# Kernel tuning notes

Hardware: AMD Instinct MI355X
Metric: run time of the kernel (lower is better)

The kernel has to match this reference:

```python
import math
import jax, jax.numpy as jnp
import numpy as np

NH = 16          # num_attention_heads
MAX_REL = 512    # max_relative_positions


def _t4(x):
    # [B, N, H] -> [B, NH, N, H/NH]  (transpose_for_scores)
    B, N, H = x.shape
    return x.reshape(B, N, NH, -1).transpose(0, 2, 1, 3)


def setup_inputs() -> dict:
    key = jax.random.key(0)
    ks = jax.random.split(key, 6)
    B, N, H = 1, 2048, 1024
    hidden_states = jax.random.normal(ks[0], (B, N, H), jnp.float32)
    attention_mask = jnp.ones((B, 1, N, N), jnp.int32)
    ids = jnp.arange(N, dtype=jnp.int32)
    relative_pos = ids[:, None] - ids[None, :]              # [N, N], build_relative_position
    rel_embeddings = jax.random.normal(ks[1], (2 * MAX_REL, H), jnp.float32) * 0.02
    in_proj_w = jax.random.normal(ks[2], (3 * H, H), jnp.float32) * 0.02
    q_bias = jnp.zeros((H,), jnp.float32)
    v_bias = jnp.zeros((H,), jnp.float32)
    pos_proj_w = jax.random.normal(ks[3], (H, H), jnp.float32) * 0.02
    pos_q_proj_w = jax.random.normal(ks[4], (H, H), jnp.float32) * 0.02
    pos_q_proj_b = jnp.zeros((H,), jnp.float32)
    return dict(hidden_states=hidden_states, attention_mask=attention_mask,
                relative_pos=relative_pos, rel_embeddings=rel_embeddings,
                in_proj_w=in_proj_w, q_bias=q_bias, v_bias=v_bias,
                pos_proj_w=pos_proj_w, pos_q_proj_w=pos_q_proj_w,
                pos_q_proj_b=pos_q_proj_b)


def reference(hidden_states, attention_mask, relative_pos, rel_embeddings,
              in_proj_w, q_bias, v_bias, pos_proj_w, pos_q_proj_w, pos_q_proj_b):
    B, N, H = hidden_states.shape
    dh = H // NH
    scale_factor = 1 + 2  # 1 + len(["c2p", "p2c"])
    scale = math.sqrt(dh * scale_factor)

    # fused QKV projection; chunk(3, dim=-1) AFTER transpose_for_scores -> per-head q|k|v layout
    qp = hidden_states @ in_proj_w.T                          # [B, N, 3H]
    q, k, v = jnp.split(_t4(qp), 3, axis=-1)                  # each [B, NH, N, dh]
    q = q + _t4(q_bias[None, None, :])
    v = v + _t4(v_bias[None, None, :])
    q = q / scale

    scores = jnp.einsum('bhqd,bhkd->bhqk', q, k)              # content-content

    # disentangled relative-position bias
    span = min(N, MAX_REL)                                    # att_span
    rel = rel_embeddings[MAX_REL - span:MAX_REL + span][None] # [1, 2S, H]
    rpos = relative_pos.astype(jnp.int32)[None, None]         # [1, 1, N, N]

    # c2p: content-to-position
    pos_k = _t4(rel @ pos_proj_w.T)                           # [1, NH, 2S, dh]
    c2p = jnp.einsum('bhqd,xhsd->bhqs', q, pos_k)             # [B, NH, N, 2S]
    c2p_pos = jnp.clip(rpos + span, 0, 2 * span - 1)
    c2p = jnp.take_along_axis(c2p, c2p_pos, axis=-1)          # gather -> [B, NH, N, N]

    # p2c: position-to-content
    pos_q = _t4(rel @ pos_q_proj_w.T + pos_q_proj_b) / scale  # [1, NH, 2S, dh]
    p2c = jnp.einsum('bhkd,xhsd->bhks', k, pos_q)             # [B, NH, N, 2S]
    p2c_pos = jnp.clip(-rpos + span, 0, 2 * span - 1)
    p2c = jnp.take_along_axis(p2c, p2c_pos, axis=-1)          # [B, NH, K, Q]
    p2c = jnp.swapaxes(p2c, -1, -2)                           # -> [B, NH, Q, K]

    scores = scores + c2p + p2c

    # XSoftmax: masked softmax, masked probs zeroed
    m = attention_mask.astype(bool)                           # [B, 1, N, N]
    probs = jax.nn.softmax(jnp.where(m, scores, -jnp.inf), axis=-1)
    probs = jnp.where(m, probs, 0.0)

    ctx = jnp.einsum('bhqk,bhkd->bhqd', probs, v)             # [B, NH, N, dh]
    return ctx.transpose(0, 2, 1, 3).reshape(B, N, H)
```

## Files before the change

### kernel.cpp

```cpp
#include <hip/hip_runtime.h>
#include <hip/hip_bf16.h>

typedef __bf16 bf16;
typedef __attribute__((ext_vector_type(8))) __bf16 bf16x8;
typedef __attribute__((ext_vector_type(8))) float f32x8;
typedef __attribute__((ext_vector_type(4))) float f32x4;

#define MFMA(a,b,c) __builtin_amdgcn_mfma_f32_16x16x32_bf16((a),(b),(c),0,0,0)

__device__ __forceinline__ bf16x8 ld8(const bf16* p){ bf16x8 v; __builtin_memcpy(&v,p,16); return v; }
__device__ __forceinline__ void   st8(bf16* p, bf16x8 v){ __builtin_memcpy(p,&v,16); }

__global__ __launch_bounds__(256)
void cvt_kernel(const float* __restrict__ s0, const float* __restrict__ s1,
                const float* __restrict__ s2, const float* __restrict__ s3,
                const float* __restrict__ s4,
                bf16* d0, bf16* d1, bf16* d2, bf16* d3, bf16* d4)
{
    const int sizes[5] = {2097152, 3145728, 1048576, 1048576, 1048576};
    const float* s; bf16* d;
    switch (blockIdx.y) {
        case 0: s = s0; d = d0; break;  case 1: s = s1; d = d1; break;
        case 2: s = s2; d = d2; break;  case 3: s = s3; d = d3; break;
        default: s = s4; d = d4;
    }
    const int n = sizes[blockIdx.y];
    const int stride = gridDim.x * 256 * 8;
    for (int i = (blockIdx.x * 256 + threadIdx.x) * 8; i < n; i += stride) {
        f32x8 v; __builtin_memcpy(&v, s + i, 32);
        bf16x8 r;
        #pragma unroll
        for (int j = 0; j < 8; j++) r[j] = (bf16)v[j];
        st8(d + i, r);
    }
}

__global__ __launch_bounds__(256)
void gemm_stage(const bf16* __restrict__ A, const bf16* __restrict__ Bpk,
                const bf16* __restrict__ Bpq, int K, int mode,
                const float* __restrict__ qb, const float* __restrict__ vb,
                bf16* __restrict__ o0, bf16* __restrict__ o1, bf16* __restrict__ o2,
                float* __restrict__ part)
{
    __shared__ __attribute__((aligned(16))) bf16 As[128][32];
    __shared__ __attribute__((aligned(16))) bf16 Bs[128][32];

    const int tid = threadIdx.x, w = tid >> 6, lane = tid & 63;
    const int l15 = lane & 15, quad = lane >> 4;
    const int wr = w >> 1, wc = w & 1;

    int arr = 0, my = blockIdx.y, kbeg = 0, kend = K;
    const bf16* B = Bpk;
    if (mode == 1) {
        arr = my >> 3; my &= 7;
        B = arr ? Bpq : Bpk;
        kbeg = blockIdx.z * 256; kend = kbeg + 256;
    }
    const int m0 = my * 128, n0 = blockIdx.x * 128;
    const int srow = tid >> 2, scol = (tid & 3) * 8;

    f32x4 acc[4][4] = {};
    for (int k0 = kbeg; k0 < kend; k0 += 32) {
        __syncthreads();
        st8(&As[srow][scol],    ld8(A + (size_t)(m0 + srow) * K + k0 + scol));
        st8(&As[srow+64][scol], ld8(A + (size_t)(m0 + 64 + srow) * K + k0 + scol));
        st8(&Bs[srow][scol],    ld8(B + (size_t)(n0 + srow) * K + k0 + scol));
        st8(&Bs[srow+64][scol], ld8(B + (size_t)(n0 + 64 + srow) * K + k0 + scol));
        __syncthreads();
        bf16x8 a[4], b[4];
        #pragma unroll
        for (int i = 0; i < 4; i++) a[i] = ld8(&As[wr*64 + i*16 + l15][quad*8]);
        #pragma unroll
        for (int j = 0; j < 4; j++) b[j] = ld8(&Bs[wc*64 + j*16 + l15][quad*8]);
        #pragma unroll
        for (int i = 0; i < 4; i++)
            #pragma unroll
            for (int j = 0; j < 4; j++)
                acc[i][j] = MFMA(a[i], b[j], acc[i][j]);
    }

    const float inv_scale = 0.07216878364870323f;
    #pragma unroll
    for (int i = 0; i < 4; i++) {
        #pragma unroll
        for (int j = 0; j < 4; j++) {
            #pragma unroll
            for (int r = 0; r < 4; r++) {
                int row = m0 + wr*64 + i*16 + quad*4 + r;
                int col = n0 + wc*64 + j*16 + l15;
                float v = acc[i][j][r];
                if (mode == 0) {
                    int h = col / 192, rr = col % 192;
                    if (rr < 64)
                        o0[((size_t)h*2048 + row)*64 + rr] =
                            (bf16)((v + qb[h*64 + rr]) * inv_scale);
                    else if (rr < 128)
                        o1[((size_t)h*2048 + row)*64 + (rr - 64)] = (bf16)v;
                    else
                        o2[((size_t)h*64 + (rr - 128))*2048 + row] =
                            (bf16)(v + vb[h*64 + (rr - 128)]);
                } else {
                    part[(((size_t)(arr*4 + blockIdx.z)*1024 + row)*1024) + col] = v;
                }
            }
        }
    }
}

__global__ __launch_bounds__(256)
void pos_merge(const float* __restrict__ part, const float* __restrict__ pqb,
               bf16* __restrict__ PKw, bf16* __restrict__ PQw)
{
    int e = blockIdx.x * 256 + threadIdx.x;
    int arr = e >> 20, r = (e >> 10) & 1023, c = e & 1023;
    const float* p = part + ((size_t)arr*4) * 1048576 + (size_t)r * 1024 + c;
    float v = p[0] + p[1048576] + p[2*1048576] + p[3*1048576];
    int h = c >> 6, d = c & 63;
    if (arr == 0) PKw[((size_t)h*1024 + r)*64 + d] = (bf16)v;
    else          PQw[((size_t)h*1024 + r)*64 + d] =
                      (bf16)((v + pqb[c]) * 0.07216878364870323f);
}

__global__ __launch_bounds__(256)
void edge_kernel(const bf16* __restrict__ Qw, const bf16* __restrict__ Kw,
                 const bf16* __restrict__ PKw, const bf16* __restrict__ PQw,
                 float* __restrict__ C2Pe, float* __restrict__ P2Ce)
{
    int t = blockIdx.x * 256 + threadIdx.x;
    int side = t >> 15, rest = t & 32767;
    int h = rest >> 11, n = rest & 2047;
    const bf16* row = (side ? Kw : Qw) + ((size_t)h*2048 + n) * 64;
    const bf16* eb  = (side ? PQw : PKw) + (size_t)h*1024*64;
    float a0 = 0.f, a1 = 0.f;
    #pragma unroll
    for (int c = 0; c < 8; c++) {
        bf16x8 x  = ld8(row + c*8);
        bf16x8 e0 = ld8(eb + c*8);
        bf16x8 e1 = ld8(eb + (size_t)1023*64 + c*8);
        #pragma unroll
        for (int j = 0; j < 8; j++) {
            a0 += (float)x[j] * (float)e0[j];
            a1 += (float)x[j] * (float)e1[j];
        }
    }
    float* o = side ? P2Ce : C2Pe;
    o[((size_t)h*2048 + n)*2 + 0] = a0;
    o[((size_t)h*2048 + n)*2 + 1] = a1;
}

__global__ __launch_bounds__(64, 2)
void attn_kernel(const bf16* __restrict__ Q, const bf16* __restrict__ Kc,
                 const bf16* __restrict__ Vt, const bf16* __restrict__ PK,
                 const bf16* __restrict__ PQ,
                 const float* __restrict__ C2Pe, const float* __restrict__ P2Ce,
                 float* __restrict__ out)
{
    __shared__ bf16 W1s[16][82];
    __shared__ bf16 W2s[64][82];
    __shared__ __attribute__((aligned(16))) bf16 Ps[16][72];

    const int lane = threadIdx.x;
    const int l15 = lane & 15, quad = lane >> 4;
    const int h = blockIdx.y, qw0 = blockIdx.x * 16;

    const bf16* Qh  = Q  + (size_t)h * 2048 * 64;
    const bf16* Kh  = Kc + (size_t)h * 2048 * 64;
    const bf16* Vh  = Vt + (size_t)h * 64 * 2048;
    const bf16* PKh = PK + (size_t)h * 1024 * 64;
    const bf16* PQh = PQ + (size_t)h * 1024 * 64;

    bf16x8 qa[2];
    #pragma unroll
    for (int s = 0; s < 2; s++)
        qa[s] = ld8(Qh + (size_t)(qw0 + l15)*64 + s*32 + quad*8);

    float c2pe0[4], c2pe1[4];
    #pragma unroll
    for (int r = 0; r < 4; r++) {
        int q = qw0 + quad*4 + r;
        c2pe0[r] = C2Pe[((size_t)h*2048 + q)*2 + 0];
        c2pe1[r] = C2Pe[((size_t)h*2048 + q)*2 + 1];
    }

    f32x4 oacc[4] = {};
    float psum[4] = {0.f, 0.f, 0.f, 0.f};

    for (int kb = 0; kb < 32; kb++) {
        const int k0 = kb * 64;

        bf16x8 kf[4][2];
        #pragma unroll
        for (int nt = 0; nt < 4; nt++)
            #pragma unroll
            for (int s = 0; s < 2; s++)
                kf[nt][s] = ld8(Kh + (size_t)(k0 + nt*16 + l15)*64 + s*32 + quad*8);

        f32x4 sacc[4] = {};
        #pragma unroll
        for (int s = 0; s < 2; s++)
            #pragma unroll
            for (int nt = 0; nt < 4; nt++)
                sacc[nt] = MFMA(qa[s], kf[nt][s], sacc[nt]);

        float val[4][4];
        if (k0 >= qw0 + 527) {
            float p2[4];
            #pragma unroll
            for (int nt = 0; nt < 4; nt++)
                p2[nt] = P2Ce[((size_t)h*2048 + k0 + nt*16 + l15)*2 + 0];
            #pragma unroll
            for (int nt = 0; nt < 4; nt++)
                #pragma unroll
                for (int r = 0; r < 4; r++)
                    val[nt][r] = sacc[nt][r] + c2pe0[r] + p2[nt];
        } else if (k0 <= qw0 - 574) {
            float p2[4];
            #pragma unroll
            for (int nt = 0; nt < 4; nt++)
                p2[nt] = P2Ce[((size_t)h*2048 + k0 + nt*16 + l15)*2 + 1];
            #pragma unroll
            for (int nt = 0; nt < 4; nt++)
                #pragma unroll
                for (int r = 0; r < 4; r++)
                    val[nt][r] = sacc[nt][r] + c2pe1[r] + p2[nt];
        } else {
            const int winb = qw0 - k0 + 449;
            {
                f32x4 a1[5] = {};
                #pragma unroll
                for (int s = 0; s < 2; s++)
                    #pragma unroll
                    for (int n5 = 0; n5 < 5; n5++) {
                        int c = winb + n5*16 + l15;
                        c = min(max(c, 0), 1023);
                        bf16x8 bq = ld8(PKh + (size_t)c*64 + s*32 + quad*8);
                        a1[n5] = MFMA(qa[s], bq, a1[n5]);
                    }
                #pragma unroll
                for (int n5 = 0; n5 < 5; n5++)
                    #pragma unroll
                    for (int r = 0; r < 4; r++)
                        W1s[quad*4 + r][n5*16 + l15] = (bf16)a1[n5][r];
            }
            {
                bf16x8 pq[5][2];
                #pragma unroll
                for (int s = 0; s < 2; s++)
                    #pragma unroll
                    for (int n5 = 0; n5 < 5; n5++) {
                        int c = winb + n5*16 + l15;
                        c = min(max(c, 0), 1023);
                        pq[n5][s] = ld8(PQh + (size_t)c*64 + s*32 + quad*8);
                    }
                #pragma unroll
                for (int mt = 0; mt < 4; mt++) {
                    f32x4 a2[5] = {};
                    #pragma unroll
                    for (int s = 0; s < 2; s++)
                        #pragma unroll
                        for (int n5 = 0; n5 < 5; n5++)
                            a2[n5] = MFMA(kf[mt][s], pq[n5][s], a2[n5]);
                    #pragma unroll
                    for (int n5 = 0; n5 < 5; n5++)
                        #pragma unroll
                        for (int r = 0; r < 4; r++)
                            W2s[mt*16 + quad*4 + r][n5*16 + l15] = (bf16)a2[n5][r];
                }
            }
            #pragma unroll
            for (int nt = 0; nt < 4; nt++)
                #pragma unroll
                for (int r = 0; r < 4; r++) {
                    int off = quad*4 + r - nt*16 - l15 + 63;
                    val[nt][r] = sacc[nt][r] + (float)W1s[quad*4 + r][off]
                                             + (float)W2s[nt*16 + l15][off];
                }
        }

        #pragma unroll
        for (int nt = 0; nt < 4; nt++)
            #pragma unroll
            for (int r = 0; r < 4; r++) {
                float e = __expf(val[nt][r]);
                psum[r] += e;
                Ps[quad*4 + r][nt*16 + l15] = (bf16)e;
            }

        #pragma unroll
        for (int s = 0; s < 2; s++) {
            bf16x8 pa = ld8(&Ps[l15][s*32 + quad*8]);
            #pragma unroll
            for (int dt = 0; dt < 4; dt++) {
                bf16x8 vf = ld8(Vh + (size_t)(dt*16 + l15)*2048 + k0 + s*32 + quad*8);
                oacc[dt] = MFMA(pa, vf, oacc[dt]);
            }
        }
    }

    #pragma unroll
    for (int r = 0; r < 4; r++)
        #pragma unroll
        for (int m = 1; m < 16; m <<= 1)
            psum[r] += __shfl_xor(psum[r], m);
    #pragma unroll
    for (int dt = 0; dt < 4; dt++)
        #pragma unroll
        for (int r = 0; r < 4; r++) {
            int row = qw0 + quad*4 + r;
            out[(size_t)row*1024 + h*64 + dt*16 + l15] = oacc[dt][r] / psum[r];
        }
}

extern "C" void kernel_launch(void* const* d_in, const int* in_sizes, int n_in,
                              void* d_out, int out_size, void* d_ws, size_t ws_size,
                              hipStream_t stream)
{
    (void)in_sizes; (void)n_in; (void)out_size; (void)ws_size;
    const float* X   = (const float*)d_in[0];
    const float* REL = (const float*)d_in[3];
    const float* Win = (const float*)d_in[4];
    const float* qb  = (const float*)d_in[5];
    const float* vb  = (const float*)d_in[6];
    const float* Wpk = (const float*)d_in[7];
    const float* Wpq = (const float*)d_in[8];
    const float* pqb = (const float*)d_in[9];
    float* out = (float*)d_out;

    char* ws = (char*)d_ws;
    const size_t MB = 1024u * 1024u;
    bf16*  Xb    = (bf16*)(ws);
    bf16*  Winb  = (bf16*)(ws + 4*MB);
    bf16*  Wpkb  = (bf16*)(ws + 10*MB);
    bf16*  Wpqb  = (bf16*)(ws + 12*MB);
    bf16*  RELb  = (bf16*)(ws + 14*MB);
    bf16*  Qw    = (bf16*)(ws + 16*MB);
    bf16*  Kw    = (bf16*)(ws + 20*MB);
    bf16*  Vtw   = (bf16*)(ws + 24*MB);
    bf16*  PKw   = (bf16*)(ws + 28*MB);
    bf16*  PQw   = (bf16*)(ws + 30*MB);
    float* Ppart = (float*)(ws + 32*MB);
    float* C2Pe  = (float*)(ws + 64*MB);
    float* P2Ce  = (float*)(ws + 64*MB + 256*1024);

    cvt_kernel<<<dim3(1536, 5), 256, 0, stream>>>(X, Win, Wpk, Wpq, REL,
                                                  Xb, Winb, Wpkb, Wpqb, RELb);
    gemm_stage<<<dim3(24, 16, 1), 256, 0, stream>>>(Xb, Winb, Winb, 1024, 0,
                                                    qb, vb, Qw, Kw, Vtw, nullptr);
    gemm_stage<<<dim3(8, 16, 4), 256, 0, stream>>>(RELb, Wpkb, Wpqb, 1024, 1,
                                                   nullptr, nullptr,
                                                   nullptr, nullptr, nullptr, Ppart);
    pos_merge<<<dim3(8192), 256, 0, stream>>>(Ppart, pqb, PKw, PQw);
    edge_kernel<<<dim3(256), 256, 0, stream>>>(Qw, Kw, PKw, PQw, C2Pe, P2Ce);
    attn_kernel<<<dim3(128, 16), 64, 0, stream>>>(Qw, Kw, Vtw, PKw, PQw,
                                                  C2Pe, P2Ce, out);
}
```

Measured before the change: 368.9 us.

## Fuse fp32-to-bf16 conversion into GEMM loads and split attention over key halves

Drops the separate conversion kernel; the GEMMs now read fp32 inputs and convert to bf16 while staging into shared memory. The attention kernel is split into two key-range halves (grid z=2) that write partial outputs and row sums, which a new merge kernel adds and normalizes. It also halves the W2s shared buffer by computing the p2c window in two halves and raises the occupancy hint. The split doubles the number of workgroups to fill more CUs, at the cost of extra partial-result traffic and a further launch. The GEMMs now read twice as many bytes per tile.

```diff
diff --git a/kernel.cpp b/kernel.cpp
--- a/kernel.cpp
+++ b/kernel.cpp
@@ -10,34 +10,17 @@
 
 __device__ __forceinline__ bf16x8 ld8(const bf16* p){ bf16x8 v; __builtin_memcpy(&v,p,16); return v; }
 __device__ __forceinline__ void   st8(bf16* p, bf16x8 v){ __builtin_memcpy(p,&v,16); }
+__device__ __forceinline__ bf16x8 ld8f(const float* p) {
+    f32x8 v; __builtin_memcpy(&v, p, 32);
+    bf16x8 r;
+    #pragma unroll
+    for (int i = 0; i < 8; i++) r[i] = (bf16)v[i];
+    return r;
+}
 
 __global__ __launch_bounds__(256)
-void cvt_kernel(const float* __restrict__ s0, const float* __restrict__ s1,
-                const float* __restrict__ s2, const float* __restrict__ s3,
-                const float* __restrict__ s4,
-                bf16* d0, bf16* d1, bf16* d2, bf16* d3, bf16* d4)
-{
-    const int sizes[5] = {2097152, 3145728, 1048576, 1048576, 1048576};
-    const float* s; bf16* d;
-    switch (blockIdx.y) {
-        case 0: s = s0; d = d0; break;  case 1: s = s1; d = d1; break;
-        case 2: s = s2; d = d2; break;  case 3: s = s3; d = d3; break;
-        default: s = s4; d = d4;
-    }
-    const int n = sizes[blockIdx.y];
-    const int stride = gridDim.x * 256 * 8;
-    for (int i = (blockIdx.x * 256 + threadIdx.x) * 8; i < n; i += stride) {
-        f32x8 v; __builtin_memcpy(&v, s + i, 32);
-        bf16x8 r;
-        #pragma unroll
-        for (int j = 0; j < 8; j++) r[j] = (bf16)v[j];
-        st8(d + i, r);
-    }
-}
-
-__global__ __launch_bounds__(256)
-void gemm_stage(const bf16* __restrict__ A, const bf16* __restrict__ Bpk,
-                const bf16* __restrict__ Bpq, int K, int mode,
+void gemm_stage(const float* __restrict__ A, const float* __restrict__ Bpk,
+                const float* __restrict__ Bpq, int K, int mode,
                 const float* __restrict__ qb, const float* __restrict__ vb,
                 bf16* __restrict__ o0, bf16* __restrict__ o1, bf16* __restrict__ o2,
                 float* __restrict__ part)
@@ -50,7 +33,7 @@
     const int wr = w >> 1, wc = w & 1;
 
     int arr = 0, my = blockIdx.y, kbeg = 0, kend = K;
-    const bf16* B = Bpk;
+    const float* B = Bpk;
     if (mode == 1) {
         arr = my >> 3; my &= 7;
         B = arr ? Bpq : Bpk;
@@ -62,10 +45,10 @@
     f32x4 acc[4][4] = {};
     for (int k0 = kbeg; k0 < kend; k0 += 32) {
         __syncthreads();
-        st8(&As[srow][scol],    ld8(A + (size_t)(m0 + srow) * K + k0 + scol));
-        st8(&As[srow+64][scol], ld8(A + (size_t)(m0 + 64 + srow) * K + k0 + scol));
-        st8(&Bs[srow][scol],    ld8(B + (size_t)(n0 + srow) * K + k0 + scol));
-        st8(&Bs[srow+64][scol], ld8(B + (size_t)(n0 + 64 + srow) * K + k0 + scol));
+        st8(&As[srow][scol],    ld8f(A + (size_t)(m0 + srow) * K + k0 + scol));
+        st8(&As[srow+64][scol], ld8f(A + (size_t)(m0 + 64 + srow) * K + k0 + scol));
+        st8(&Bs[srow][scol],    ld8f(B + (size_t)(n0 + srow) * K + k0 + scol));
+        st8(&Bs[srow+64][scol], ld8f(B + (size_t)(n0 + 64 + srow) * K + k0 + scol));
         __syncthreads();
         bf16x8 a[4], b[4];
         #pragma unroll
@@ -148,20 +131,21 @@
     o[((size_t)h*2048 + n)*2 + 1] = a1;
 }
 
-__global__ __launch_bounds__(64, 2)
+__global__ __launch_bounds__(64, 4)
 void attn_kernel(const bf16* __restrict__ Q, const bf16* __restrict__ Kc,
                  const bf16* __restrict__ Vt, const bf16* __restrict__ PK,
                  const bf16* __restrict__ PQ,
                  const float* __restrict__ C2Pe, const float* __restrict__ P2Ce,
-                 float* __restrict__ out)
+                 float* __restrict__ Opart, float* __restrict__ Lpart)
 {
     __shared__ bf16 W1s[16][82];
-    __shared__ bf16 W2s[64][82];
+    __shared__ bf16 W2s[32][82];
     __shared__ __attribute__((aligned(16))) bf16 Ps[16][72];
 
     const int lane = threadIdx.x;
     const int l15 = lane & 15, quad = lane >> 4;
     const int h = blockIdx.y, qw0 = blockIdx.x * 16;
+    const int split = blockIdx.z;
 
     const bf16* Qh  = Q  + (size_t)h * 2048 * 64;
     const bf16* Kh  = Kc + (size_t)h * 2048 * 64;
@@ -185,7 +169,8 @@
     f32x4 oacc[4] = {};
     float psum[4] = {0.f, 0.f, 0.f, 0.f};
 
-    for (int kb = 0; kb < 32; kb++) {
+    const int kb0 = split * 16;
+    for (int kb = kb0; kb < kb0 + 16; kb++) {
         const int k0 = kb * 64;
 
         bf16x8 kf[4][2];
@@ -242,18 +227,20 @@
                     for (int r = 0; r < 4; r++)
                         W1s[quad*4 + r][n5*16 + l15] = (bf16)a1[n5][r];
             }
-            {
-                bf16x8 pq[5][2];
-                #pragma unroll
-                for (int s = 0; s < 2; s++)
-                    #pragma unroll
-                    for (int n5 = 0; n5 < 5; n5++) {
-                        int c = winb + n5*16 + l15;
-                        c = min(max(c, 0), 1023);
-                        pq[n5][s] = ld8(PQh + (size_t)c*64 + s*32 + quad*8);
-                    }
-                #pragma unroll
-                for (int mt = 0; mt < 4; mt++) {
+            bf16x8 pq[5][2];
+            #pragma unroll
+            for (int s = 0; s < 2; s++)
+                #pragma unroll
+                for (int n5 = 0; n5 < 5; n5++) {
+                    int c = winb + n5*16 + l15;
+                    c = min(max(c, 0), 1023);
+                    pq[n5][s] = ld8(PQh + (size_t)c*64 + s*32 + quad*8);
+                }
+            #pragma unroll
+            for (int half = 0; half < 2; half++) {
+                #pragma unroll
+                for (int mtl = 0; mtl < 2; mtl++) {
+                    const int mt = half*2 + mtl;
                     f32x4 a2[5] = {};
                     #pragma unroll
                     for (int s = 0; s < 2; s++)
@@ -264,17 +251,19 @@
                     for (int n5 = 0; n5 < 5; n5++)
                         #pragma unroll
                         for (int r = 0; r < 4; r++)
-                            W2s[mt*16 + quad*4 + r][n5*16 + l15] = (bf16)a2[n5][r];
+                            W2s[mtl*16 + quad*4 + r][n5*16 + l15] = (bf16)a2[n5][r];
                 }
-            }
-            #pragma unroll
-            for (int nt = 0; nt < 4; nt++)
-                #pragma unroll
-                for (int r = 0; r < 4; r++) {
-                    int off = quad*4 + r - nt*16 - l15 + 63;
-                    val[nt][r] = sacc[nt][r] + (float)W1s[quad*4 + r][off]
-                                             + (float)W2s[nt*16 + l15][off];
+                #pragma unroll
+                for (int ntl = 0; ntl < 2; ntl++) {
+                    const int nt = half*2 + ntl;
+                    #pragma unroll
+                    for (int r = 0; r < 4; r++) {
+                        int off = quad*4 + r - nt*16 - l15 + 63;
+                        val[nt][r] = sacc[nt][r] + (float)W1s[quad*4 + r][off]
+                                                 + (float)W2s[ntl*16 + l15][off];
+                    }
                 }
+            }
         }
 
         #pragma unroll
@@ -302,13 +291,32 @@
         #pragma unroll
         for (int m = 1; m < 16; m <<= 1)
             psum[r] += __shfl_xor(psum[r], m);
+
+    const size_t pb = (size_t)((split << 4) + h);
     #pragma unroll
     for (int dt = 0; dt < 4; dt++)
         #pragma unroll
         for (int r = 0; r < 4; r++) {
             int row = qw0 + quad*4 + r;
-            out[(size_t)row*1024 + h*64 + dt*16 + l15] = oacc[dt][r] / psum[r];
-        }
+            Opart[(pb*2048 + row)*64 + dt*16 + l15] = oacc[dt][r];
+        }
+    if (l15 == 0)
+        #pragma unroll
+        for (int r = 0; r < 4; r++)
+            Lpart[pb*2048 + qw0 + quad*4 + r] = psum[r];
+}
+
+__global__ __launch_bounds__(256)
+void attn_merge(const float* __restrict__ Opart, const float* __restrict__ Lpart,
+                float* __restrict__ out)
+{
+    int e = blockIdx.x * 256 + threadIdx.x;
+    int row = e >> 10, c = e & 1023;
+    int h = c >> 6, d = c & 63;
+    float o = Opart[((size_t)h*2048 + row)*64 + d]
+            + Opart[(((size_t)16 + h)*2048 + row)*64 + d];
+    float l = Lpart[(size_t)h*2048 + row] + Lpart[((size_t)16 + h)*2048 + row];
+    out[e] = o / l;
 }
 
 extern "C" void kernel_launch(void* const* d_in, const int* in_sizes, int n_in,
@@ -328,29 +336,25 @@
 
     char* ws = (char*)d_ws;
     const size_t MB = 1024u * 1024u;
-    bf16*  Xb    = (bf16*)(ws);
-    bf16*  Winb  = (bf16*)(ws + 4*MB);
-    bf16*  Wpkb  = (bf16*)(ws + 10*MB);
-    bf16*  Wpqb  = (bf16*)(ws + 12*MB);
-    bf16*  RELb  = (bf16*)(ws + 14*MB);
-    bf16*  Qw    = (bf16*)(ws + 16*MB);
-    bf16*  Kw    = (bf16*)(ws + 20*MB);
-    bf16*  Vtw   = (bf16*)(ws + 24*MB);
-    bf16*  PKw   = (bf16*)(ws + 28*MB);
-    bf16*  PQw   = (bf16*)(ws + 30*MB);
-    float* Ppart = (float*)(ws + 32*MB);
-    float* C2Pe  = (float*)(ws + 64*MB);
-    float* P2Ce  = (float*)(ws + 64*MB + 256*1024);
-
-    cvt_kernel<<<dim3(1536, 5), 256, 0, stream>>>(X, Win, Wpk, Wpq, REL,
-                                                  Xb, Winb, Wpkb, Wpqb, RELb);
-    gemm_stage<<<dim3(24, 16, 1), 256, 0, stream>>>(Xb, Winb, Winb, 1024, 0,
+    bf16*  Qw    = (bf16*)(ws);
+    bf16*  Kw    = (bf16*)(ws + 4*MB);
+    bf16*  Vtw   = (bf16*)(ws + 8*MB);
+    bf16*  PKw   = (bf16*)(ws + 12*MB);
+    bf16*  PQw   = (bf16*)(ws + 14*MB);
+    float* Ppart = (float*)(ws + 16*MB);
+    float* Opart = (float*)(ws + 16*MB);
+    float* Lpart = (float*)(ws + 32*MB);
+    float* C2Pe  = (float*)(ws + 48*MB);
+    float* P2Ce  = (float*)(ws + 48*MB + 256*1024);
+
+    gemm_stage<<<dim3(24, 16, 1), 256, 0, stream>>>(X, Win, Win, 1024, 0,
                                                     qb, vb, Qw, Kw, Vtw, nullptr);
-    gemm_stage<<<dim3(8, 16, 4), 256, 0, stream>>>(RELb, Wpkb, Wpqb, 1024, 1,
+    gemm_stage<<<dim3(8, 16, 4), 256, 0, stream>>>(REL, Wpk, Wpq, 1024, 1,
                                                    nullptr, nullptr,
                                                    nullptr, nullptr, nullptr, Ppart);
     pos_merge<<<dim3(8192), 256, 0, stream>>>(Ppart, pqb, PKw, PQw);
     edge_kernel<<<dim3(256), 256, 0, stream>>>(Qw, Kw, PKw, PQw, C2Pe, P2Ce);
-    attn_kernel<<<dim3(128, 16), 64, 0, stream>>>(Qw, Kw, Vtw, PKw, PQw,
-                                                  C2Pe, P2Ce, out);
-}
+    attn_kernel<<<dim3(128, 16, 2), 64, 0, stream>>>(Qw, Kw, Vtw, PKw, PQw,
+                                                     C2Pe, P2Ce, Opart, Lpart);
+    attn_merge<<<dim3(8192), 256, 0, stream>>>(Opart, Lpart, out);
+}
```

Measured after the change: 493.9 us. +33.9%, slower.
